# Kernel optimization log

Measured on AMD Instinct MI355X. Metric: run time of the kernel, lower is better.

## Reference

```python
import jax, jax.numpy as jnp
import numpy as np

B, T, IN, H, F = 512, 32, 8, 64, 1
IN1 = IN + F  # input_size + feats


def setup_inputs() -> dict:
    key = jax.random.key(0)
    ks = jax.random.split(key, 8)
    s = 0.05
    return {
        "input_data": jax.random.normal(ks[0], (B, T, IN), jnp.float32),
        "y_prev": jax.random.normal(ks[1], (B, T), jnp.float32),
        "Wv": jax.random.normal(ks[2], (H, H + IN1), jnp.float32) * s,
        "bv": jnp.zeros((H,), jnp.float32),
        "W_ih": jax.random.normal(ks[3], (4 * H, IN1), jnp.float32) * s,
        "W_hh": jax.random.normal(ks[4], (4 * H, H), jnp.float32) * s,
        "b_ih": jnp.zeros((4 * H,), jnp.float32),
        "b_hh": jnp.zeros((4 * H,), jnp.float32),
        "Wp": jax.random.normal(ks[5], (1, H + IN1), jnp.float32) * s,
        "bp": jnp.zeros((1,), jnp.float32),
        "Wf": jax.random.normal(ks[6], (F, H), jnp.float32) * s,
        "bf": jnp.zeros((F,), jnp.float32),
        "num_particles": 256,
    }


def _forward(input_data, y_prev, Wv, bv, W_ih, W_hh, b_ih, b_hh, Wp, bp, Wf, bf, num_particles):
    b, t_len, _ = input_data.shape
    h_dim = Wf.shape[1]
    P = num_particles
    noise_key = jax.random.key(1234)

    new_input = jnp.concatenate([input_data, y_prev[:, :, None]], axis=2)  # [B,T,IN1]
    xs = jnp.moveaxis(new_input, 1, 0)  # [T,B,IN1]
    h0 = jnp.zeros((P, b, h_dim), input_data.dtype)
    c0 = jnp.zeros((P, b, h_dim), input_data.dtype)

    def step(carry, xt_t):
        h, c = carry  # each [P,B,H], particle-major
        x_t, t = xt_t  # [B,IN1], scalar t
        hidden_mean = h.mean(axis=0)  # [B,H] (mean over particles)
        var = jnp.concatenate([x_t, hidden_mean], axis=1) @ Wv.T + bv  # [B,H]
        std = jax.nn.softplus(var)
        # single LSTM cell step over P*B "batch" rows (input tiled over particles)
        gates = x_t @ W_ih.T + b_ih + h @ W_hh.T + b_hh  # [P,B,4H]
        i, f, g, o = jnp.split(gates, 4, axis=-1)  # torch gate order i,f,g,o
        c_new = jax.nn.sigmoid(f) * c + jax.nn.sigmoid(i) * jnp.tanh(g)
        h_lstm = jax.nn.sigmoid(o) * jnp.tanh(c_new)
        # reparameterize: mu + eps*std (std broadcast over particle dim)
        eps = jax.random.normal(jax.random.fold_in(noise_key, t), (P, b, h_dim), h.dtype)
        h_rep = h_lstm + eps * std
        # sort_hidden: per batch element, reorder particles by fc_final projection
        proj = (h_rep @ Wf.T + bf)[..., 0]  # [P,B]
        order = jnp.argsort(proj, axis=0)  # [P,B]
        h_sorted = jnp.take_along_axis(h_rep, order[:, :, None], axis=0)
        y = jnp.concatenate([h_sorted, jnp.broadcast_to(x_t, (P, b, x_t.shape[1]))], axis=-1)
        logpdf = (y @ Wp.T + bp)[..., 0]  # [P,B]
        # faithful to torch's view(-1, P, 1) on a particle-major flat buffer
        pr = logpdf.reshape(-1).reshape(b, P)
        w_inc = jnp.exp(pr).mean(axis=1, keepdims=True)  # [B,1]
        return (h_sorted, c_new), w_inc

    (h_fin, _), w_incs = jax.lax.scan(step, (h0, c0), (xs, jnp.arange(t_len)))
    weights = w_incs.sum(axis=0)  # [B,1]
    y_pred = h_fin.mean(axis=0) @ Wf.T + bf  # [B,1]
    return y_pred, weights


def reference(input_data, y_prev, Wv, bv, W_ih, W_hh, b_ih, b_hh, Wp, bp, Wf, bf, num_particles):
    return _forward(input_data, y_prev, Wv, bv, W_ih, W_hh, b_ih, b_hh, Wp, bp, Wf, bf, num_particles)
```

## Files before the change

kernel.cpp:

```cpp
#include <hip/hip_runtime.h>
#include <stdint.h>

#define NB 512
#define NT 32
#define NIN 8
#define NIN1 9
#define NH 64
#define NP 256
#define NTHR 512
#define HROW 68

typedef __attribute__((ext_vector_type(8))) _Float16 f16x8;
typedef __attribute__((ext_vector_type(4))) float f32x4;

struct FKeys { uint32_t a[NT]; uint32_t b[NT]; };

__host__ __device__ __forceinline__ void tfr(uint32_t& x0, uint32_t& x1, int r) {
  x0 += x1; x1 = (x1 << r) | (x1 >> (32 - r)); x1 ^= x0;
}

__host__ __device__ __forceinline__ void threefry2x32(uint32_t k0, uint32_t k1,
                                                      uint32_t& x0, uint32_t& x1) {
  uint32_t k2 = k0 ^ k1 ^ 0x1BD11BDAu;
  x0 += k0; x1 += k1;
  tfr(x0,x1,13); tfr(x0,x1,15); tfr(x0,x1,26); tfr(x0,x1,6);
  x0 += k1; x1 += k2 + 1u;
  tfr(x0,x1,17); tfr(x0,x1,29); tfr(x0,x1,16); tfr(x0,x1,24);
  x0 += k2; x1 += k0 + 2u;
  tfr(x0,x1,13); tfr(x0,x1,15); tfr(x0,x1,26); tfr(x0,x1,6);
  x0 += k0; x1 += k1 + 3u;
  tfr(x0,x1,17); tfr(x0,x1,29); tfr(x0,x1,16); tfr(x0,x1,24);
  x0 += k1; x1 += k2 + 4u;
  tfr(x0,x1,13); tfr(x0,x1,15); tfr(x0,x1,26); tfr(x0,x1,6);
  x0 += k2; x1 += k0 + 5u;
}

__device__ __forceinline__ float normal_from_bits(uint32_t bits) {
  float f = __uint_as_float((bits >> 9) | 0x3f800000u) - 1.0f;
  const float lo = -0.99999994f;
  float u = fmaxf(lo, fmaf(f, 2.0f, lo));
  float w = -__logf(fmaf(-u, u, 1.0f));
  float p;
  if (w < 5.0f) {
    w -= 2.5f;
    p = 2.81022636e-08f;
    p = fmaf(p, w, 3.43273939e-07f);
    p = fmaf(p, w, -3.5233877e-06f);
    p = fmaf(p, w, -4.39150654e-06f);
    p = fmaf(p, w, 0.00021858087f);
    p = fmaf(p, w, -0.00125372503f);
    p = fmaf(p, w, -0.00417768164f);
    p = fmaf(p, w, 0.246640727f);
    p = fmaf(p, w, 1.50140941f);
  } else {
    w = sqrtf(w) - 3.0f;
    p = -0.000200214257f;
    p = fmaf(p, w, 0.000100950558f);
    p = fmaf(p, w, 0.00134934322f);
    p = fmaf(p, w, -0.00367342844f);
    p = fmaf(p, w, 0.00573950773f);
    p = fmaf(p, w, -0.0076224613f);
    p = fmaf(p, w, 0.00943887047f);
    p = fmaf(p, w, 1.00167406f);
    p = fmaf(p, w, 2.83297682f);
  }
  return 1.41421356f * (p * u);
}

__device__ __forceinline__ float frcp(float x) { return __builtin_amdgcn_rcpf(x); }
__device__ __forceinline__ float fsigmoid(float x) { return frcp(1.0f + __expf(-x)); }
__device__ __forceinline__ float ftanh(float x) { return 1.0f - 2.0f * frcp(1.0f + __expf(2.0f * x)); }

__device__ __forceinline__ uint32_t pack_f16(float x) {
  union { _Float16 h; uint16_t u; } c;
  c.h = (_Float16)x;
  return (uint32_t)c.u;
}
__device__ __forceinline__ float unpk_f16(uint32_t w, int hi) {
  union { _Float16 h; uint16_t u; } c;
  c.u = hi ? (uint16_t)(w >> 16) : (uint16_t)(w & 0xffffu);
  return (float)c.h;
}

__device__ __forceinline__ f16x8 ld8h(const _Float16* p) {
  union { f16x8 v; uint64_t q[2]; } u;
  u.q[0] = *(const uint64_t*)(p);
  u.q[1] = *(const uint64_t*)(p + 4);
  return u.v;
}

__global__ __launch_bounds__(NTHR, 2)
void pf_main(const float* __restrict__ input_data, const float* __restrict__ y_prev,
             const float* __restrict__ Wv, const float* __restrict__ bv,
             const float* __restrict__ W_ih, const float* __restrict__ W_hh,
             const float* __restrict__ b_ih, const float* __restrict__ b_hh,
             const float* __restrict__ Wp, const float* __restrict__ bp,
             const float* __restrict__ Wf, const float* __restrict__ bf,
             float* __restrict__ out, float* __restrict__ gw,
             FKeys fk)
{
  __shared__ __align__(16) _Float16 h1_s[NP * HROW];
  __shared__ __align__(16) _Float16 h0_s[NP * HROW];
  __shared__ __align__(16) float xg_s[NP];
  __shared__ __align__(16) float proj_s[NP];
  __shared__ float lp_s[NP];
  __shared__ float wsum_s[NP];
  __shared__ int   rankP_s[2 * NP];
  __shared__ float hsum_s[NH];
  __shared__ float std_s[NH];
  __shared__ float xs_s[16];

  const int tid  = threadIdx.x;
  const int b    = blockIdx.x;
  const int lane = tid & 63;
  const int wq   = tid >> 6;
  const int lrow = (lane >> 4) & 3;
  const int lcol = lane & 15;

  for (int i = tid; i < NP * HROW; i += NTHR) h1_s[i] = (_Float16)0.0f;
  if (tid < NP) wsum_s[tid] = 0.0f;
  if (tid < NH) hsum_s[tid] = 0.0f;

  const float bf0 = bf[0];
  const float bp0 = bp[0];
  const uint32_t bsh = (uint32_t)b << 6;

  f16x8 w1f[2][2];
  #pragma unroll
  for (int kg2 = 0; kg2 < 2; ++kg2) {
    const int rpr  = 32 * wq + 16 * kg2 + lcol;
    const int orig = (rpr & 3) * NH + (rpr >> 2);
    #pragma unroll
    for (int kt = 0; kt < 2; ++kt) {
      #pragma unroll
      for (int e = 0; e < 8; ++e)
        w1f[kg2][kt][e] = (_Float16)W_hh[orig * NH + kt * 32 + lrow * 8 + e];
    }
  }

  float wf2[2], wp2[2];
  #pragma unroll
  for (int kg2 = 0; kg2 < 2; ++kg2) {
    const int k = 8 * wq + 4 * kg2 + lrow;
    wf2[kg2] = Wf[k];
    wp2[kg2] = Wp[k];
  }

  uint32_t cp[2][8];
  #pragma unroll
  for (int kg2 = 0; kg2 < 2; ++kg2)
    #pragma unroll
    for (int j = 0; j < 8; ++j) cp[kg2][j] = 0u;

  auto finalize_init = [&]() {
    if (tid < NH) {
      float v = bv[tid];
      const float* wvr = Wv + tid * (NIN1 + NH);
      #pragma unroll
      for (int i = 0; i < NIN1; ++i) v = fmaf(xs_s[i], wvr[i], v);
      #pragma unroll
      for (int k = 0; k < NH; ++k)
        v = fmaf(hsum_s[k] * (1.0f / NP), wvr[NIN1 + k], v);
      std_s[tid] = fmaxf(v, 0.0f) + log1pf(expf(-fabsf(v)));
    }
    if (tid < NP) {
      const int orow = (tid & 3) * NH + (tid >> 2);
      float a = b_ih[orow] + b_hh[orow];
      const float* wr = W_ih + orow * NIN1;
      #pragma unroll
      for (int i = 0; i < NIN1; ++i) a = fmaf(xs_s[i], wr[i], a);
      xg_s[tid] = a;
      proj_s[tid] = bf0;
      float xp = bp0;
      #pragma unroll
      for (int i = 0; i < NIN1; ++i) xp = fmaf(xs_s[i], Wp[NH + i], xp);
      lp_s[tid] = xp;
    }
  };

  if (tid < NIN) xs_s[tid] = input_data[(b * NT + 0) * NIN + tid];
  if (tid == NIN) xs_s[NIN] = y_prev[b * NT + 0];
  __syncthreads();
  finalize_init();
  __syncthreads();

  for (int t = 0; t < NT; ++t) {
    if (tid < 16 && t + 1 < NT) {
      if (tid < NIN) xs_s[tid] = input_data[(b * NT + t + 1) * NIN + tid];
      if (tid == NIN) xs_s[NIN] = y_prev[b * NT + t + 1];
    }

    float std2[2];
    #pragma unroll
    for (int kg2 = 0; kg2 < 2; ++kg2) std2[kg2] = std_s[8 * wq + 4 * kg2 + lrow];

    const uint32_t fk0 = fk.a[t], fk1 = fk.b[t];
    float hs2[2] = {0.0f, 0.0f};

    #pragma unroll
    for (int pt8 = 0; pt8 < 8; ++pt8) {
      const int p = 16 * pt8 + lcol;
      const f16x8 bA0 = ld8h(&h1_s[p * HROW + lrow * 8]);
      const f16x8 bA1 = ld8h(&h1_s[p * HROW + 32 + lrow * 8]);
      const f16x8 bB0 = ld8h(&h1_s[(p + 128) * HROW + lrow * 8]);
      const f16x8 bB1 = ld8h(&h1_s[(p + 128) * HROW + 32 + lrow * 8]);

      float plp = 0.0f, lpp = 0.0f, plp1 = 0.0f, lpp1 = 0.0f;
      #pragma unroll
      for (int kg2 = 0; kg2 < 2; ++kg2) {
        const int k = 8 * wq + 4 * kg2 + lrow;
        const float4 xgv = *(const float4*)&xg_s[32 * wq + 16 * kg2 + 4 * lrow];
        f32x4 accA, accB;
        accA[0] = xgv.x; accA[1] = xgv.y; accA[2] = xgv.z; accA[3] = xgv.w;
        accB = accA;
        accA = __builtin_amdgcn_mfma_f32_16x16x32_f16(w1f[kg2][0], bA0, accA, 0, 0, 0);
        accB = __builtin_amdgcn_mfma_f32_16x16x32_f16(w1f[kg2][0], bB0, accB, 0, 0, 0);
        accA = __builtin_amdgcn_mfma_f32_16x16x32_f16(w1f[kg2][1], bA1, accA, 0, 0, 0);
        accB = __builtin_amdgcn_mfma_f32_16x16x32_f16(w1f[kg2][1], bB1, accB, 0, 0, 0);
        float si = fsigmoid(accA[0]);
        float sf = fsigmoid(accA[1]);
        float so = fsigmoid(accA[3]);
        float cold = unpk_f16(cp[kg2][pt8], 0);
        float cn = sf * cold + si * ftanh(accA[2]);
        float hlA = so * ftanh(cn);
        float si2 = fsigmoid(accB[0]);
        float sf2 = fsigmoid(accB[1]);
        float so2 = fsigmoid(accB[3]);
        float cold2 = unpk_f16(cp[kg2][pt8], 1);
        float cn2 = sf2 * cold2 + si2 * ftanh(accB[2]);
        cp[kg2][pt8] = pack_f16(cn) | (pack_f16(cn2) << 16);
        float hlB = so2 * ftanh(cn2);
        uint32_t x0 = ((uint32_t)p << 15) | bsh | (uint32_t)k;
        uint32_t x1 = x0 + (1u << 22);
        threefry2x32(fk0, fk1, x0, x1);
        float hA = fmaf(normal_from_bits(x0), std2[kg2], hlA);
        float hB = fmaf(normal_from_bits(x1), std2[kg2], hlB);
        hs2[kg2] += hA + hB;
        plp  = fmaf(hA, wf2[kg2], plp);  lpp  = fmaf(hA, wp2[kg2], lpp);
        plp1 = fmaf(hB, wf2[kg2], plp1); lpp1 = fmaf(hB, wp2[kg2], lpp1);
        h0_s[p * HROW + k] = (_Float16)hA;
        h0_s[(p + 128) * HROW + k] = (_Float16)hB;
      }
      plp  += __shfl_xor(plp, 16, 64);  plp  += __shfl_xor(plp, 32, 64);
      lpp  += __shfl_xor(lpp, 16, 64);  lpp  += __shfl_xor(lpp, 32, 64);
      plp1 += __shfl_xor(plp1, 16, 64); plp1 += __shfl_xor(plp1, 32, 64);
      lpp1 += __shfl_xor(lpp1, 16, 64); lpp1 += __shfl_xor(lpp1, 32, 64);
      if (lane < 16) {
        atomicAdd(&proj_s[p], plp);
        atomicAdd(&lp_s[p], lpp);
        atomicAdd(&proj_s[p + 128], plp1);
        atomicAdd(&lp_s[p + 128], lpp1);
      }
    }
    #pragma unroll
    for (int kg2 = 0; kg2 < 2; ++kg2) {
      float s = hs2[kg2];
      s += __shfl_xor(s, 1, 64); s += __shfl_xor(s, 2, 64);
      s += __shfl_xor(s, 4, 64); s += __shfl_xor(s, 8, 64);
      if (lcol == 0) hsum_s[8 * wq + 4 * kg2 + lrow] = s;
    }
    __syncthreads();

    {
      const int ph = tid & (NP - 1);
      const int hh = tid >> 8;
      const float pv = proj_s[ph];
      int rk = 0;
      const float4* c4 = (const float4*)proj_s;
      #pragma unroll 8
      for (int q4 = 32 * hh; q4 < 32 * hh + 32; ++q4) {
        float4 v = c4[q4];
        int qb = q4 * 4;
        rk += (v.x < pv || (v.x == pv && qb + 0 < ph)) ? 1 : 0;
        rk += (v.y < pv || (v.y == pv && qb + 1 < ph)) ? 1 : 0;
        rk += (v.z < pv || (v.z == pv && qb + 2 < ph)) ? 1 : 0;
        rk += (v.w < pv || (v.w == pv && qb + 3 < ph)) ? 1 : 0;
      }
      rankP_s[hh * NP + ph] = rk;
    }
    __syncthreads();

    {
      const int ph = tid & (NP - 1);
      const int hh = tid >> 8;
      const int rank = rankP_s[ph] + rankP_s[NP + ph];
      const uint64_t* s = (const uint64_t*)&h0_s[ph * HROW + 32 * hh];
      const uint64_t v0 = s[0], v1 = s[1], v2 = s[2], v3 = s[3];
      uint64_t* d = (uint64_t*)&h1_s[rank * HROW + 32 * hh];
      d[0] = v0; d[1] = v1; d[2] = v2; d[3] = v3;
      if (hh == 0) wsum_s[rank] += __expf(lp_s[ph]);
    }
    finalize_init();
    __syncthreads();
  }

  if (tid < NH) {
    float hm = hsum_s[tid] * (1.0f / NP);
    float contrib = hm * Wf[tid];
    contrib += __shfl_xor(contrib, 32, 64);
    contrib += __shfl_xor(contrib, 16, 64);
    contrib += __shfl_xor(contrib, 8, 64);
    contrib += __shfl_xor(contrib, 4, 64);
    contrib += __shfl_xor(contrib, 2, 64);
    contrib += __shfl_xor(contrib, 1, 64);
    if (tid == 0) out[b] = contrib + bf0;
  }
  if (tid < NP) gw[(size_t)tid * NB + b] = wsum_s[tid];
}

__global__ __launch_bounds__(64, 1)
void pf_weights(const float* __restrict__ gw, float* __restrict__ out) {
  int i = blockIdx.x;
  int lane = threadIdx.x;
  const float* src = gw + ((size_t)(i >> 1)) * NB + (size_t)(i & 1) * NP;
  float4 v = ((const float4*)src)[lane];
  float s = (v.x + v.y) + (v.z + v.w);
  s += __shfl_xor(s, 32, 64);
  s += __shfl_xor(s, 16, 64);
  s += __shfl_xor(s, 8, 64);
  s += __shfl_xor(s, 4, 64);
  s += __shfl_xor(s, 2, 64);
  s += __shfl_xor(s, 1, 64);
  if (lane == 0) out[NB + i] = s * (1.0f / NP);
}

extern "C" void kernel_launch(void* const* d_in, const int* in_sizes, int n_in,
                              void* d_out, int out_size, void* d_ws, size_t ws_size,
                              hipStream_t stream) {
  (void)in_sizes; (void)n_in; (void)out_size; (void)ws_size;
  const float* input_data = (const float*)d_in[0];
  const float* y_prev     = (const float*)d_in[1];
  const float* Wv         = (const float*)d_in[2];
  const float* bv         = (const float*)d_in[3];
  const float* W_ih       = (const float*)d_in[4];
  const float* W_hh       = (const float*)d_in[5];
  const float* b_ih       = (const float*)d_in[6];
  const float* b_hh       = (const float*)d_in[7];
  const float* Wp         = (const float*)d_in[8];
  const float* bp         = (const float*)d_in[9];
  const float* Wf         = (const float*)d_in[10];
  const float* bf         = (const float*)d_in[11];
  float* out = (float*)d_out;
  float* gw  = (float*)d_ws;

  FKeys fk;
  for (int t = 0; t < NT; ++t) {
    uint32_t x0 = 0u, x1 = (uint32_t)t;
    threefry2x32(0u, 1234u, x0, x1);
    fk.a[t] = x0; fk.b[t] = x1;
  }

  pf_main<<<dim3(NB), dim3(NTHR), 0, stream>>>(
      input_data, y_prev, Wv, bv, W_ih, W_hh, b_ih, b_hh, Wp, bp, Wf, bf,
      out, gw, fk);
  pf_weights<<<dim3(NB), dim3(64), 0, stream>>>(gw, out);
}
```

Measured before the change: 1.343 ms.

## Move cell state to global memory and scatter hidden rows directly from registers

The LSTM cell state, previously packed as fp16 in registers, is now kept in fp32 in a global workspace and read and written every step. The h0_s shared staging buffer is removed: new hidden values stay packed in registers and are scattered straight into their sorted rows of h1_s after ranking. This halves the shared-memory footprint, which may allow more blocks per CU, and drops one LDS round-trip. The cost is extra global traffic on every step and scattered 2-byte LDS writes.

```diff
diff --git a/kernel.cpp b/kernel.cpp
--- a/kernel.cpp
+++ b/kernel.cpp
@@ -76,10 +76,10 @@
   c.h = (_Float16)x;
   return (uint32_t)c.u;
 }
-__device__ __forceinline__ float unpk_f16(uint32_t w, int hi) {
+__device__ __forceinline__ _Float16 bits_to_h(uint16_t u) {
   union { _Float16 h; uint16_t u; } c;
-  c.u = hi ? (uint16_t)(w >> 16) : (uint16_t)(w & 0xffffu);
-  return (float)c.h;
+  c.u = u;
+  return c.h;
 }
 
 __device__ __forceinline__ f16x8 ld8h(const _Float16* p) {
@@ -96,11 +96,10 @@
              const float* __restrict__ b_ih, const float* __restrict__ b_hh,
              const float* __restrict__ Wp, const float* __restrict__ bp,
              const float* __restrict__ Wf, const float* __restrict__ bf,
-             float* __restrict__ out, float* __restrict__ gw,
+             float* __restrict__ out, float* __restrict__ gw, float* __restrict__ cg,
              FKeys fk)
 {
   __shared__ __align__(16) _Float16 h1_s[NP * HROW];
-  __shared__ __align__(16) _Float16 h0_s[NP * HROW];
   __shared__ __align__(16) float xg_s[NP];
   __shared__ __align__(16) float proj_s[NP];
   __shared__ float lp_s[NP];
@@ -146,11 +145,7 @@
     wp2[kg2] = Wp[k];
   }
 
-  uint32_t cp[2][8];
-  #pragma unroll
-  for (int kg2 = 0; kg2 < 2; ++kg2)
-    #pragma unroll
-    for (int j = 0; j < 8; ++j) cp[kg2][j] = 0u;
+  float* cgw = cg + ((size_t)b * 8 + wq) * (2 * 8 * 128) + lane;
 
   auto finalize_init = [&]() {
     if (tid < NH) {
@@ -195,7 +190,9 @@
     for (int kg2 = 0; kg2 < 2; ++kg2) std2[kg2] = std_s[8 * wq + 4 * kg2 + lrow];
 
     const uint32_t fk0 = fk.a[t], fk1 = fk.b[t];
+    const bool t0 = (t == 0);
     float hs2[2] = {0.0f, 0.0f};
+    uint32_t shp[2][8];
 
     #pragma unroll
     for (int pt8 = 0; pt8 < 8; ++pt8) {
@@ -209,6 +206,9 @@
       #pragma unroll
       for (int kg2 = 0; kg2 < 2; ++kg2) {
         const int k = 8 * wq + 4 * kg2 + lrow;
+        float* cptr = cgw + (size_t)(kg2 * 8 + pt8) * 128;
+        const float cvA = cptr[0];
+        const float cvB = cptr[64];
         const float4 xgv = *(const float4*)&xg_s[32 * wq + 16 * kg2 + 4 * lrow];
         f32x4 accA, accB;
         accA[0] = xgv.x; accA[1] = xgv.y; accA[2] = xgv.z; accA[3] = xgv.w;
@@ -220,15 +220,14 @@
         float si = fsigmoid(accA[0]);
         float sf = fsigmoid(accA[1]);
         float so = fsigmoid(accA[3]);
-        float cold = unpk_f16(cp[kg2][pt8], 0);
-        float cn = sf * cold + si * ftanh(accA[2]);
+        float cn = sf * (t0 ? 0.0f : cvA) + si * ftanh(accA[2]);
+        cptr[0] = cn;
         float hlA = so * ftanh(cn);
         float si2 = fsigmoid(accB[0]);
         float sf2 = fsigmoid(accB[1]);
         float so2 = fsigmoid(accB[3]);
-        float cold2 = unpk_f16(cp[kg2][pt8], 1);
-        float cn2 = sf2 * cold2 + si2 * ftanh(accB[2]);
-        cp[kg2][pt8] = pack_f16(cn) | (pack_f16(cn2) << 16);
+        float cn2 = sf2 * (t0 ? 0.0f : cvB) + si2 * ftanh(accB[2]);
+        cptr[64] = cn2;
         float hlB = so2 * ftanh(cn2);
         uint32_t x0 = ((uint32_t)p << 15) | bsh | (uint32_t)k;
         uint32_t x1 = x0 + (1u << 22);
@@ -238,8 +237,7 @@
         hs2[kg2] += hA + hB;
         plp  = fmaf(hA, wf2[kg2], plp);  lpp  = fmaf(hA, wp2[kg2], lpp);
         plp1 = fmaf(hB, wf2[kg2], plp1); lpp1 = fmaf(hB, wp2[kg2], lpp1);
-        h0_s[p * HROW + k] = (_Float16)hA;
-        h0_s[(p + 128) * HROW + k] = (_Float16)hB;
+        shp[kg2][pt8] = pack_f16(hA) | (pack_f16(hB) << 16);
       }
       plp  += __shfl_xor(plp, 16, 64);  plp  += __shfl_xor(plp, 32, 64);
       lpp  += __shfl_xor(lpp, 16, 64);  lpp  += __shfl_xor(lpp, 32, 64);
@@ -280,15 +278,22 @@
     }
     __syncthreads();
 
-    {
-      const int ph = tid & (NP - 1);
-      const int hh = tid >> 8;
-      const int rank = rankP_s[ph] + rankP_s[NP + ph];
-      const uint64_t* s = (const uint64_t*)&h0_s[ph * HROW + 32 * hh];
-      const uint64_t v0 = s[0], v1 = s[1], v2 = s[2], v3 = s[3];
-      uint64_t* d = (uint64_t*)&h1_s[rank * HROW + 32 * hh];
-      d[0] = v0; d[1] = v1; d[2] = v2; d[3] = v3;
-      if (hh == 0) wsum_s[rank] += __expf(lp_s[ph]);
+    if (tid < NP) {
+      const int rank = rankP_s[tid] + rankP_s[NP + tid];
+      wsum_s[rank] += __expf(lp_s[tid]);
+    }
+    #pragma unroll
+    for (int kg2 = 0; kg2 < 2; ++kg2) {
+      const int k = 8 * wq + 4 * kg2 + lrow;
+      #pragma unroll
+      for (int pt8 = 0; pt8 < 8; ++pt8) {
+        const int p = 16 * pt8 + lcol;
+        const int rA = rankP_s[p] + rankP_s[NP + p];
+        const int rB = rankP_s[p + 128] + rankP_s[NP + p + 128];
+        const uint32_t v = shp[kg2][pt8];
+        h1_s[rA * HROW + k] = bits_to_h((uint16_t)(v & 0xffffu));
+        h1_s[rB * HROW + k] = bits_to_h((uint16_t)(v >> 16));
+      }
     }
     finalize_init();
     __syncthreads();
@@ -342,6 +347,7 @@
   const float* bf         = (const float*)d_in[11];
   float* out = (float*)d_out;
   float* gw  = (float*)d_ws;
+  float* cg  = gw + (size_t)NP * NB;
 
   FKeys fk;
   for (int t = 0; t < NT; ++t) {
@@ -352,6 +358,6 @@
 
   pf_main<<<dim3(NB), dim3(NTHR), 0, stream>>>(
       input_data, y_prev, Wv, bv, W_ih, W_hh, b_ih, b_hh, Wp, bp, Wf, bf,
-      out, gw, fk);
+      out, gw, cg, fk);
   pf_weights<<<dim3(NB), dim3(64), 0, stream>>>(gw, out);
 }
```

New measurement: 1.336 ms. Within noise of the previous version (-0.5%).
